# Performance work log

Hardware: AMD Instinct MI355X
Metric: run time of the kernel (lower is better)

Reference implementation:

```python
import jax, jax.numpy as jnp
import numpy as np

# NTU-25 joint groupings (0-indexed)
BODY_GROUP = [np.array([5,6,7,8,22,23])-1, np.array([9,10,11,12,24,25])-1,
              np.array([13,14,15,16])-1, np.array([17,18,19,20])-1,
              np.array([1,2,3,4,21])-1]
PART_GROUP = [np.array([1,2,21])-1, np.array([3,4])-1, np.array([5,6,7])-1,
              np.array([8,22,23])-1, np.array([9,10,11])-1, np.array([12,24,25])-1,
              np.array([13,14])-1, np.array([15,16])-1, np.array([17,18])-1,
              np.array([19,20])-1]

def _corr_joints(parts):
    num_joints = max(max(p) for p in parts) + 1
    res = []
    for i in range(num_joints):
        for j, p in enumerate(parts):
            if i in p:
                res.append(j)
                break
    return np.asarray(res, dtype=np.int32)

JOINTS_PART = _corr_joints(PART_GROUP)  # [25] -> part id in [0,10)
JOINTS_BODY = _corr_joints(BODY_GROUP)  # [25] -> body id in [0,5)

N, C, T, V, S = 64, 96, 128, 25, 3

def setup_inputs() -> dict:
    key = jax.random.key(0)
    ks = jax.random.split(key, 10)
    x = jax.random.normal(ks[0], (N, C, T, V), jnp.float32)
    p_att = jax.random.normal(ks[1], (N, S, 10, 10), jnp.float32)
    b_att = jax.random.normal(ks[2], (N, S, 5, 5), jnp.float32)
    w_in = jax.random.normal(ks[3], (3 * C, C), jnp.float32) * (1.0 / np.sqrt(C))
    b_in = jax.random.normal(ks[4], (3 * C,), jnp.float32) * 0.01
    w_ff = jax.random.normal(ks[5], (C, C), jnp.float32) * (1.0 / np.sqrt(C))
    b_ff = jax.random.normal(ks[6], (C,), jnp.float32) * 0.01
    bn_gamma = jnp.ones((C,), jnp.float32)
    bn_beta = jnp.zeros((C,), jnp.float32)
    bn_mean = jnp.zeros((C,), jnp.float32)
    bn_var = jnp.ones((C,), jnp.float32)
    return {"x": x, "p_att": p_att, "b_att": b_att, "w_in": w_in, "b_in": b_in,
            "w_ff": w_ff, "b_ff": b_ff, "bn_gamma": bn_gamma, "bn_beta": bn_beta,
            "bn_mean": bn_mean, "bn_var": bn_var}

def reference(x, p_att, b_att, w_in, b_in, w_ff, b_ff, bn_gamma, bn_beta, bn_mean, bn_var):
    n, c, t, v = x.shape
    s = S
    mid = c // s
    jp = jnp.asarray(JOINTS_PART)
    jb = jnp.asarray(JOINTS_BODY)
    # 1x1 conv -> QKV: [N, 3C, T, V] viewed as [N, 3, S, mid, T, V]
    qkv = jnp.einsum('nctv,oc->notv', x, w_in) + b_in[None, :, None, None]
    qkv = qkv.reshape(n, 3, s, mid, t, v)
    q, k, val = qkv[:, 0], qkv[:, 1], qkv[:, 2]
    att = jnp.tanh(jnp.einsum('nsctu,nsctv->nsuv', q, k) / (mid * t))
    # structured gather of part/body biases to joint-level [N,S,V,V]
    pp = p_att[:, :, jp[:, None], jp[None, :]]
    bb = b_att[:, :, jb[:, None], jb[None, :]]
    att = att + pp + bb
    y = jnp.einsum('nsuv,nsctv->nsctu', att, val).reshape(n, c, t, v)
    # ff_nets: 1x1 conv + BatchNorm (eval mode, running stats)
    y = jnp.einsum('nctv,oc->notv', y, w_ff) + b_ff[None, :, None, None]
    inv = bn_gamma / jnp.sqrt(bn_var + 1e-5)
    y = (y - bn_mean[None, :, None, None]) * inv[None, :, None, None] + bn_beta[None, :, None, None]
    return jax.nn.leaky_relu(x + y, 0.1)
```

## Files before the change

kernel.cpp:

```cpp
#include <hip/hip_runtime.h>
#include <cmath>

#define NN 64
#define CC 96
#define TT 128
#define VV 25
#define SS 3
#define TB 4
#define NTB (TT/TB)
#define ROWS (TB*VV)
#define XTROWS 112

#define XTP 104
#define XFP 104
#define QKP 200
#define VP  132
#define YP  104

typedef __attribute__((ext_vector_type(8))) __bf16 bf16x8;
typedef __attribute__((ext_vector_type(4))) float f32x4;

#define MFMA16(a,b,c) __builtin_amdgcn_mfma_f32_16x16x32_bf16((a),(b),(c),0,0,0)

__constant__ int JP[25] = {0,0,1,1,2,2,2,3,4,4,4,5,6,6,7,7,8,8,9,9,0,3,3,5,5};
__constant__ int JB[25] = {4,4,4,4,0,0,0,0,1,1,1,1,2,2,2,2,3,3,3,3,4,0,0,1,1};

__device__ inline unsigned short f2b(float f) {
  unsigned int u = __float_as_uint(f);
  u += 0x7fffu + ((u >> 16) & 1u);
  return (unsigned short)(u >> 16);
}
__device__ inline bf16x8 ldbf8(const unsigned short* p) {
  union { uint4 u; bf16x8 b; } z;
  z.u = *(const uint4*)p;
  return z.b;
}
__device__ inline f32x4 fz() {
  f32x4 z; z[0] = 0.f; z[1] = 0.f; z[2] = 0.f; z[3] = 0.f; return z;
}

__global__ __launch_bounds__(256) void k0(
    const float* __restrict__ w_in, const float* __restrict__ w_ff,
    const float* __restrict__ b_ff, const float* __restrict__ gam,
    const float* __restrict__ bet, const float* __restrict__ mea,
    const float* __restrict__ var,
    unsigned short* __restrict__ wbin, unsigned short* __restrict__ wbff,
    float* __restrict__ scsh)
{
  int i = blockIdx.x * 256 + threadIdx.x;
  if (i < 288 * 96) wbin[i] = f2b(w_in[i]);
  if (i < 96 * 96)  wbff[i] = f2b(w_ff[i]);
  if (i < 96) {
    float sc = gam[i] * rsqrtf(var[i] + 1e-5f);
    scsh[i]      = sc;
    scsh[96 + i] = (b_ff[i] - mea[i]) * sc + bet[i];
  }
}

__device__ inline void stageA(const float* __restrict__ xb,
                              unsigned short* __restrict__ xf, int tid)
{
  for (int e = tid; e < CC * (ROWS / 4); e += 256) {
    int i4 = e % (ROWS / 4), c = e / (ROWS / 4);
    float4 v = *(const float4*)&xb[(size_t)c * (TT * VV) + i4 * 4];
    ushort4 h;
    h.x = f2b(v.x); h.y = f2b(v.y); h.z = f2b(v.z); h.w = f2b(v.w);
    *(ushort4*)&xf[c * XFP + i4 * 4] = h;
  }
}
__device__ inline void stageB(const unsigned short* __restrict__ xf,
                              unsigned short* __restrict__ xT,
                              unsigned short* __restrict__ xwp, int tid)
{
  for (int e = tid; e < ROWS * (CC / 4); e += 256) {
    int i = e % ROWS, c4 = e / ROWS;
    ushort4 h;
    h.x = xf[(c4 * 4 + 0) * XFP + i];
    h.y = xf[(c4 * 4 + 1) * XFP + i];
    h.z = xf[(c4 * 4 + 2) * XFP + i];
    h.w = xf[(c4 * 4 + 3) * XFP + i];
    *(ushort4*)&xT[i * XTP + c4 * 4] = h;
    int dt = i / VV, v = i - dt * VV;
    *(ushort4*)&xwp[(size_t)(dt * 32 + v) * 96 + c4 * 4] = h;
  }
}

__global__ __launch_bounds__(256, 2) void k1(
    const float* __restrict__ x, const unsigned short* __restrict__ wbin,
    const float* __restrict__ b_in, float* __restrict__ partG,
    unsigned short* __restrict__ xw)
{
  __shared__ __align__(16) unsigned short xT[XTROWS * XTP];
  __shared__ __align__(16) unsigned short qk[XTROWS * QKP];
  __shared__ float bL[192];
  unsigned short* xf = qk;

  const int tid  = threadIdx.x;
  const int wid  = tid >> 6, lane = tid & 63;
  const int lrow = lane & 15;
  const int lk8  = (lane >> 4) << 3;
  const int ldr4 = (lane >> 4) << 2;
  const int tb = blockIdx.x & (NTB - 1);
  const int n  = blockIdx.x >> 5;
  const int t0 = tb * TB;

  const float* xb = x + (size_t)n * CC * TT * VV + (size_t)t0 * VV;
  unsigned short* xwp = xw + (size_t)(n * TT + t0) * 32 * 96;

  stageA(xb, xf, tid);
  if (tid < 192) bL[tid] = b_in[tid];
  __syncthreads();
  stageB(xf, xT, xwp, tid);
  __syncthreads();

  f32x4 acc[3][7];
  #pragma unroll
  for (int i = 0; i < 3; ++i)
    #pragma unroll
    for (int nf = 0; nf < 7; ++nf) acc[i][nf] = fz();

  #pragma unroll
  for (int ks = 0; ks < 3; ++ks) {
    bf16x8 a[3];
    #pragma unroll
    for (int i = 0; i < 3; ++i)
      a[i] = ldbf8(&wbin[((wid * 3 + i) * 16 + lrow) * 96 + ks * 32 + lk8]);
    #pragma unroll
    for (int nf = 0; nf < 7; ++nf) {
      bf16x8 b = ldbf8(&xT[(nf * 16 + lrow) * XTP + ks * 32 + lk8]);
      #pragma unroll
      for (int i = 0; i < 3; ++i)
        acc[i][nf] = MFMA16(a[i], b, acc[i][nf]);
    }
  }
  #pragma unroll
  for (int i = 0; i < 3; ++i) {
    int ob = (wid * 3 + i) * 16 + ldr4;
    float4 bb = *(const float4*)&bL[ob];
    #pragma unroll
    for (int nf = 0; nf < 7; ++nf) {
      int col = nf * 16 + lrow;
      ushort4 h;
      h.x = f2b(acc[i][nf][0] + bb.x);
      h.y = f2b(acc[i][nf][1] + bb.y);
      h.z = f2b(acc[i][nf][2] + bb.z);
      h.w = f2b(acc[i][nf][3] + bb.w);
      *(ushort4*)&qk[col * QKP + ob] = h;
    }
  }
  __syncthreads();

  if (wid < 3) {
    const int s = wid;
    f32x4 g[2][2];
    g[0][0] = fz(); g[0][1] = fz(); g[1][0] = fz(); g[1][1] = fz();
    #pragma unroll
    for (int dt = 0; dt < TB; ++dt) {
      int r0 = dt * VV;
      bf16x8 a0 = ldbf8(&qk[(r0 + lrow) * QKP + s * 32 + lk8]);
      bf16x8 a1 = ldbf8(&qk[(r0 + 16 + lrow) * QKP + s * 32 + lk8]);
      bf16x8 b0 = ldbf8(&qk[(r0 + lrow) * QKP + 96 + s * 32 + lk8]);
      bf16x8 b1 = ldbf8(&qk[(r0 + 16 + lrow) * QKP + 96 + s * 32 + lk8]);
      g[0][0] = MFMA16(a0, b0, g[0][0]);
      g[0][1] = MFMA16(a0, b1, g[0][1]);
      g[1][0] = MFMA16(a1, b0, g[1][0]);
      g[1][1] = MFMA16(a1, b1, g[1][1]);
    }
    float* pg = partG + ((size_t)tb * (NN * SS) + (n * SS + s)) * (VV * VV);
    #pragma unroll
    for (int mi = 0; mi < 2; ++mi)
      #pragma unroll
      for (int ni = 0; ni < 2; ++ni)
        #pragma unroll
        for (int r = 0; r < 4; ++r) {
          int u = mi * 16 + ldr4 + r, v = ni * 16 + lrow;
          if (u < VV && v < VV) pg[u * VV + v] = g[mi][ni][r];
        }
  }
}

__global__ __launch_bounds__(256) void k2(
    const float* __restrict__ partG, const float* __restrict__ p_att,
    const float* __restrict__ b_att, unsigned short* __restrict__ att)
{
  const int ns = blockIdx.x;
  for (int e = threadIdx.x; e < 1024; e += 256) {
    int u = e >> 5, v = e & 31;
    float a = 0.f;
    if (u < VV && v < VV) {
      float g = 0.f;
      #pragma unroll 4
      for (int tb = 0; tb < NTB; ++tb)
        g += partG[((size_t)tb * (NN * SS) + ns) * (VV * VV) + u * VV + v];
      a = tanhf(g * (1.0f / 4096.0f))
        + p_att[(size_t)ns * 100 + JP[u] * 10 + JP[v]]
        + b_att[(size_t)ns * 25  + JB[u] * 5  + JB[v]];
    }
    att[(size_t)ns * 1024 + e] = f2b(a);
  }
}

__global__ __launch_bounds__(256, 2) void k3(
    const float* __restrict__ x, const unsigned short* __restrict__ xw,
    const unsigned short* __restrict__ wbin,
    const unsigned short* __restrict__ wbff,
    const float* __restrict__ b_in, const float* __restrict__ scsh,
    const unsigned short* __restrict__ att, float* __restrict__ out)
{
  __shared__ __align__(16) unsigned short val[96 * VP];
  unsigned short* yL = val;

  const int tid  = threadIdx.x;
  const int wid  = tid >> 6, lane = tid & 63;
  const int lrow = lane & 15;
  const int lk8  = (lane >> 4) << 3;
  const int ldr4 = (lane >> 4) << 2;
  const int tb = blockIdx.x & (NTB - 1);
  const int n  = blockIdx.x >> 5;
  const int t0 = tb * TB;

  const unsigned short* xwn = xw + (size_t)(n * TT + t0) * 32 * 96;

  f32x4 vacc[2][6];
  #pragma unroll
  for (int m = 0; m < 2; ++m)
    #pragma unroll
    for (int of = 0; of < 6; ++of) vacc[m][of] = fz();

  #pragma unroll
  for (int ks = 0; ks < 3; ++ks) {
    bf16x8 bw[6];
    #pragma unroll
    for (int of = 0; of < 6; ++of)
      bw[of] = ldbf8(&wbin[(192 + of * 16 + lrow) * 96 + ks * 32 + lk8]);
    #pragma unroll
    for (int m = 0; m < 2; ++m) {
      bf16x8 a = ldbf8(&xwn[(size_t)((wid + m * 4) * 16 + lrow) * 96 + ks * 32 + lk8]);
      #pragma unroll
      for (int of = 0; of < 6; ++of)
        vacc[m][of] = MFMA16(a, bw[of], vacc[m][of]);
    }
  }
  float bv[6];
  #pragma unroll
  for (int of = 0; of < 6; ++of) bv[of] = b_in[192 + of * 16 + lrow];

  #pragma unroll
  for (int m = 0; m < 2; ++m) {
    int i0 = (wid + m * 4) * 16 + ldr4;
    int v0 = i0 & 31;
    #pragma unroll
    for (int of = 0; of < 6; ++of) {
      int cout = of * 16 + lrow;
      ushort4 h;
      h.x = (v0 + 0 < VV) ? f2b(vacc[m][of][0] + bv[of]) : (unsigned short)0;
      h.y = (v0 + 1 < VV) ? f2b(vacc[m][of][1] + bv[of]) : (unsigned short)0;
      h.z = (v0 + 2 < VV) ? f2b(vacc[m][of][2] + bv[of]) : (unsigned short)0;
      h.w = (v0 + 3 < VV) ? f2b(vacc[m][of][3] + bv[of]) : (unsigned short)0;
      *(ushort4*)&val[cout * VP + i0] = h;
    }
  }
  __syncthreads();

  const unsigned short* attn = att + (size_t)n * SS * 1024;
  f32x4 pacc[3][2][2];
  #pragma unroll
  for (int s = 0; s < 3; ++s)
    #pragma unroll
    for (int mi = 0; mi < 2; ++mi)
      #pragma unroll
      for (int uf = 0; uf < 2; ++uf) pacc[s][mi][uf] = fz();

  #pragma unroll
  for (int s = 0; s < 3; ++s) {
    bf16x8 av[2], bu[2];
    #pragma unroll
    for (int mi = 0; mi < 2; ++mi)
      av[mi] = ldbf8(&val[(s * 32 + mi * 16 + lrow) * VP + wid * 32 + lk8]);
    #pragma unroll
    for (int uf = 0; uf < 2; ++uf)
      bu[uf] = ldbf8(&attn[s * 1024 + (uf * 16 + lrow) * 32 + lk8]);
    #pragma unroll
    for (int mi = 0; mi < 2; ++mi)
      #pragma unroll
      for (int uf = 0; uf < 2; ++uf)
        pacc[s][mi][uf] = MFMA16(av[mi], bu[uf], pacc[s][mi][uf]);
  }
  __syncthreads();

  #pragma unroll
  for (int s = 0; s < 3; ++s)
    #pragma unroll
    for (int mi = 0; mi < 2; ++mi)
      #pragma unroll
      for (int uf = 0; uf < 2; ++uf) {
        int u = uf * 16 + lrow;
        if (u < VV) {
          int c0 = s * 32 + mi * 16 + ldr4;
          ushort4 h;
          h.x = f2b(pacc[s][mi][uf][0]);
          h.y = f2b(pacc[s][mi][uf][1]);
          h.z = f2b(pacc[s][mi][uf][2]);
          h.w = f2b(pacc[s][mi][uf][3]);
          *(ushort4*)&yL[(wid * VV + u) * YP + c0] = h;
        }
      }
  __syncthreads();

  #pragma unroll
  for (int rep = 0; rep < 2; ++rep) {
    int nf = wid + rep * 4;
    if (nf < 7) {
      f32x4 facc[6];
      #pragma unroll
      for (int of = 0; of < 6; ++of) facc[of] = fz();
      #pragma unroll
      for (int ks = 0; ks < 3; ++ks) {
        bf16x8 by = ldbf8(&yL[(nf * 16 + lrow) * YP + ks * 32 + lk8]);
        #pragma unroll
        for (int of = 0; of < 6; ++of) {
          bf16x8 aw = ldbf8(&wbff[(of * 16 + lrow) * 96 + ks * 32 + lk8]);
          facc[of] = MFMA16(aw, by, facc[of]);
        }
      }
      int i = nf * 16 + lrow;
      if (i < ROWS) {
        size_t base = (size_t)n * CC * (TT * VV) + (size_t)t0 * VV + i;
        #pragma unroll
        for (int of = 0; of < 6; ++of) {
          int o0 = of * 16 + ldr4;
          float4 sc = *(const float4*)&scsh[o0];
          float4 sh = *(const float4*)&scsh[96 + o0];
          const float* scp = (const float*)&sc;
          const float* shp = (const float*)&sh;
          #pragma unroll
          for (int r = 0; r < 4; ++r) {
            size_t idx = base + (size_t)(o0 + r) * (TT * VV);
            float z = facc[of][r] * scp[r] + shp[r] + x[idx];
            out[idx] = (z >= 0.f) ? z : 0.1f * z;
          }
        }
      }
    }
  }
}

extern "C" void kernel_launch(void* const* d_in, const int* in_sizes, int n_in,
                              void* d_out, int out_size, void* d_ws, size_t ws_size,
                              hipStream_t stream)
{
  const float* x     = (const float*)d_in[0];
  const float* p_att = (const float*)d_in[1];
  const float* b_att = (const float*)d_in[2];
  const float* w_in  = (const float*)d_in[3];
  const float* b_in  = (const float*)d_in[4];
  const float* w_ff  = (const float*)d_in[5];
  const float* b_ff  = (const float*)d_in[6];
  const float* gam   = (const float*)d_in[7];
  const float* bet   = (const float*)d_in[8];
  const float* mea   = (const float*)d_in[9];
  const float* var   = (const float*)d_in[10];
  float* out = (float*)d_out;

  char* ws = (char*)d_ws;
  unsigned short* wbin = (unsigned short*)ws;
  unsigned short* wbff = wbin + 288 * 96;
  unsigned short* attw = wbff + 96 * 96;
  float* scsh  = (float*)(ws + 466944);
  float* partG = (float*)(ws + 467712);
  unsigned short* xw = (unsigned short*)(ws + 15827712);

  k0<<<108, 256, 0, stream>>>(w_in, w_ff, b_ff, gam, bet, mea, var,
                              wbin, wbff, scsh);
  k1<<<NN * NTB, 256, 0, stream>>>(x, wbin, b_in, partG, xw);
  k2<<<NN * SS, 256, 0, stream>>>(partG, p_att, b_att, attw);
  k3<<<NN * NTB, 256, 0, stream>>>(x, xw, wbin, wbff, b_in, scsh, attw, out);
}
```

Measured before the change: 133.0 us.

## Recompute bf16 x transpose in k3 instead of round-tripping through workspace

k1 no longer writes a padded bf16 transposed copy of x to global workspace. k3 now reloads fp32 x, converts and transposes it in LDS itself, and stages the value and feed-forward weights plus the bias and scale/shift vectors in shared memory. This removes a global write and read of the intermediate and replaces scattered global weight loads with LDS reads. In exchange k3 reads x twice and uses much more LDS per block, which may lower occupancy.

```diff
diff --git a/kernel.cpp b/kernel.cpp
--- a/kernel.cpp
+++ b/kernel.cpp
@@ -14,8 +14,10 @@
 #define XTP 104
 #define XFP 104
 #define QKP 200
-#define VP  132
+#define X3P 104
+#define VP  136
 #define YP  104
+#define WLP 104
 
 typedef __attribute__((ext_vector_type(8))) __bf16 bf16x8;
 typedef __attribute__((ext_vector_type(4))) float f32x4;
@@ -68,10 +70,29 @@
     *(ushort4*)&xf[c * XFP + i4 * 4] = h;
   }
 }
-__device__ inline void stageB(const unsigned short* __restrict__ xf,
-                              unsigned short* __restrict__ xT,
-                              unsigned short* __restrict__ xwp, int tid)
-{
+
+__global__ __launch_bounds__(256, 2) void k1(
+    const float* __restrict__ x, const unsigned short* __restrict__ wbin,
+    const float* __restrict__ b_in, float* __restrict__ partG)
+{
+  __shared__ __align__(16) unsigned short xT[XTROWS * XTP];
+  __shared__ __align__(16) unsigned short qk[XTROWS * QKP];
+  __shared__ float bL[192];
+  unsigned short* xf = qk;
+
+  const int tid  = threadIdx.x;
+  const int wid  = tid >> 6, lane = tid & 63;
+  const int lrow = lane & 15;
+  const int lk8  = (lane >> 4) << 3;
+  const int ldr4 = (lane >> 4) << 2;
+  const int tb = blockIdx.x & (NTB - 1);
+  const int n  = blockIdx.x >> 5;
+  const int t0 = tb * TB;
+
+  const float* xb = x + (size_t)n * CC * TT * VV + (size_t)t0 * VV;
+  stageA(xb, xf, tid);
+  if (tid < 192) bL[tid] = b_in[tid];
+  __syncthreads();
   for (int e = tid; e < ROWS * (CC / 4); e += 256) {
     int i = e % ROWS, c4 = e / ROWS;
     ushort4 h;
@@ -80,37 +101,7 @@
     h.z = xf[(c4 * 4 + 2) * XFP + i];
     h.w = xf[(c4 * 4 + 3) * XFP + i];
     *(ushort4*)&xT[i * XTP + c4 * 4] = h;
-    int dt = i / VV, v = i - dt * VV;
-    *(ushort4*)&xwp[(size_t)(dt * 32 + v) * 96 + c4 * 4] = h;
-  }
-}
-
-__global__ __launch_bounds__(256, 2) void k1(
-    const float* __restrict__ x, const unsigned short* __restrict__ wbin,
-    const float* __restrict__ b_in, float* __restrict__ partG,
-    unsigned short* __restrict__ xw)
-{
-  __shared__ __align__(16) unsigned short xT[XTROWS * XTP];
-  __shared__ __align__(16) unsigned short qk[XTROWS * QKP];
-  __shared__ float bL[192];
-  unsigned short* xf = qk;
-
-  const int tid  = threadIdx.x;
-  const int wid  = tid >> 6, lane = tid & 63;
-  const int lrow = lane & 15;
-  const int lk8  = (lane >> 4) << 3;
-  const int ldr4 = (lane >> 4) << 2;
-  const int tb = blockIdx.x & (NTB - 1);
-  const int n  = blockIdx.x >> 5;
-  const int t0 = tb * TB;
-
-  const float* xb = x + (size_t)n * CC * TT * VV + (size_t)t0 * VV;
-  unsigned short* xwp = xw + (size_t)(n * TT + t0) * 32 * 96;
-
-  stageA(xb, xf, tid);
-  if (tid < 192) bL[tid] = b_in[tid];
-  __syncthreads();
-  stageB(xf, xT, xwp, tid);
+  }
   __syncthreads();
 
   f32x4 acc[3][7];
@@ -201,14 +192,18 @@
 }
 
 __global__ __launch_bounds__(256, 2) void k3(
-    const float* __restrict__ x, const unsigned short* __restrict__ xw,
-    const unsigned short* __restrict__ wbin,
+    const float* __restrict__ x, const unsigned short* __restrict__ wbin,
     const unsigned short* __restrict__ wbff,
     const float* __restrict__ b_in, const float* __restrict__ scsh,
     const unsigned short* __restrict__ att, float* __restrict__ out)
 {
+  __shared__ __align__(16) unsigned short xT32[128 * X3P];
   __shared__ __align__(16) unsigned short val[96 * VP];
-  unsigned short* yL = val;
+  __shared__ __align__(16) unsigned short wL[96 * WLP];
+  __shared__ float bvL[96];
+  __shared__ float scshL[192];
+  unsigned short* xf = val;
+  unsigned short* yL = xT32;
 
   const int tid  = threadIdx.x;
   const int wid  = tid >> 6, lane = tid & 63;
@@ -219,7 +214,35 @@
   const int n  = blockIdx.x >> 5;
   const int t0 = tb * TB;
 
-  const unsigned short* xwn = xw + (size_t)(n * TT + t0) * 32 * 96;
+  const float* xb = x + (size_t)n * CC * TT * VV + (size_t)t0 * VV;
+
+  stageA(xb, xf, tid);
+  for (int e = tid; e < 96 * 12; e += 256) {
+    int r = e / 12, q = e % 12;
+    *(uint4*)&wL[r * WLP + q * 8] =
+        *(const uint4*)&wbin[(size_t)(192 + r) * 96 + q * 8];
+  }
+  for (int e = tid; e < 28 * 13; e += 256) {
+    int pr = e / 13, q = e % 13;
+    int row = (pr / 7) * 32 + 25 + (pr % 7);
+    uint4 z; z.x = 0u; z.y = 0u; z.z = 0u; z.w = 0u;
+    *(uint4*)&xT32[row * X3P + q * 8] = z;
+  }
+  if (tid < 96)  bvL[tid]   = b_in[192 + tid];
+  if (tid < 192) scshL[tid] = scsh[tid];
+  __syncthreads();
+
+  for (int e = tid; e < ROWS * (CC / 4); e += 256) {
+    int i = e % ROWS, c4 = e / ROWS;
+    int row = (i / VV) * 32 + (i % VV);
+    ushort4 h;
+    h.x = xf[(c4 * 4 + 0) * XFP + i];
+    h.y = xf[(c4 * 4 + 1) * XFP + i];
+    h.z = xf[(c4 * 4 + 2) * XFP + i];
+    h.w = xf[(c4 * 4 + 3) * XFP + i];
+    *(ushort4*)&xT32[row * X3P + c4 * 4] = h;
+  }
+  __syncthreads();
 
   f32x4 vacc[2][6];
   #pragma unroll
@@ -232,10 +255,10 @@
     bf16x8 bw[6];
     #pragma unroll
     for (int of = 0; of < 6; ++of)
-      bw[of] = ldbf8(&wbin[(192 + of * 16 + lrow) * 96 + ks * 32 + lk8]);
+      bw[of] = ldbf8(&wL[(of * 16 + lrow) * WLP + ks * 32 + lk8]);
     #pragma unroll
     for (int m = 0; m < 2; ++m) {
-      bf16x8 a = ldbf8(&xwn[(size_t)((wid + m * 4) * 16 + lrow) * 96 + ks * 32 + lk8]);
+      bf16x8 a = ldbf8(&xT32[((wid + m * 4) * 16 + lrow) * X3P + ks * 32 + lk8]);
       #pragma unroll
       for (int of = 0; of < 6; ++of)
         vacc[m][of] = MFMA16(a, bw[of], vacc[m][of]);
@@ -243,7 +266,7 @@
   }
   float bv[6];
   #pragma unroll
-  for (int of = 0; of < 6; ++of) bv[of] = b_in[192 + of * 16 + lrow];
+  for (int of = 0; of < 6; ++of) bv[of] = bvL[of * 16 + lrow];
 
   #pragma unroll
   for (int m = 0; m < 2; ++m) {
@@ -262,6 +285,12 @@
   }
   __syncthreads();
 
+  for (int e = tid; e < 96 * 12; e += 256) {
+    int r = e / 12, q = e % 12;
+    *(uint4*)&wL[r * WLP + q * 8] =
+        *(const uint4*)&wbff[(size_t)r * 96 + q * 8];
+  }
+
   const unsigned short* attn = att + (size_t)n * SS * 1024;
   f32x4 pacc[3][2][2];
   #pragma unroll
@@ -286,7 +315,6 @@
       for (int uf = 0; uf < 2; ++uf)
         pacc[s][mi][uf] = MFMA16(av[mi], bu[uf], pacc[s][mi][uf]);
   }
-  __syncthreads();
 
   #pragma unroll
   for (int s = 0; s < 3; ++s)
@@ -319,7 +347,7 @@
         bf16x8 by = ldbf8(&yL[(nf * 16 + lrow) * YP + ks * 32 + lk8]);
         #pragma unroll
         for (int of = 0; of < 6; ++of) {
-          bf16x8 aw = ldbf8(&wbff[(of * 16 + lrow) * 96 + ks * 32 + lk8]);
+          bf16x8 aw = ldbf8(&wL[(of * 16 + lrow) * WLP + ks * 32 + lk8]);
           facc[of] = MFMA16(aw, by, facc[of]);
         }
       }
@@ -329,8 +357,8 @@
         #pragma unroll
         for (int of = 0; of < 6; ++of) {
           int o0 = of * 16 + ldr4;
-          float4 sc = *(const float4*)&scsh[o0];
-          float4 sh = *(const float4*)&scsh[96 + o0];
+          float4 sc = *(const float4*)&scshL[o0];
+          float4 sh = *(const float4*)&scshL[96 + o0];
           const float* scp = (const float*)&sc;
           const float* shp = (const float*)&sh;
           #pragma unroll
@@ -368,11 +396,10 @@
   unsigned short* attw = wbff + 96 * 96;
   float* scsh  = (float*)(ws + 466944);
   float* partG = (float*)(ws + 467712);
-  unsigned short* xw = (unsigned short*)(ws + 15827712);
 
   k0<<<108, 256, 0, stream>>>(w_in, w_ff, b_ff, gam, bet, mea, var,
                               wbin, wbff, scsh);
-  k1<<<NN * NTB, 256, 0, stream>>>(x, wbin, b_in, partG, xw);
+  k1<<<NN * NTB, 256, 0, stream>>>(x, wbin, b_in, partG);
   k2<<<NN * SS, 256, 0, stream>>>(partG, p_att, b_att, attw);
-  k3<<<NN * NTB, 256, 0, stream>>>(x, xw, wbin, wbff, b_in, scsh, attw, out);
-}
+  k3<<<NN * NTB, 256, 0, stream>>>(x, wbin, wbff, b_in, scsh, attw, out);
+}
```

Result: faster. 130.1 us (-2.2%).

## Compute V projection in k1 and write bf16 values instead of transposed x

Applied to the files above, without the earlier changes.

The V projection moves from k3 into k1, which already holds x in shared memory. k1 now writes the finished bf16 V tensor, padded to 32 joints, to workspace instead of a transposed copy of x. k3 reads V straight from global memory, stages the ff weights in LDS, and raises its occupancy hint to 3 blocks. The intent is to shorten k3 and remove the repeated V GEMM there, at the cost of larger LDS use and a longer k1, where the QKV GEMM now also covers padding rows (8 fragments instead of 7).

```diff
diff --git a/kernel.cpp b/kernel.cpp
--- a/kernel.cpp
+++ b/kernel.cpp
@@ -9,13 +9,12 @@
 #define TB 4
 #define NTB (TT/TB)
 #define ROWS (TB*VV)
-#define XTROWS 112
-
-#define XTP 104
+
 #define XFP 104
+#define X3P 104
 #define QKP 200
-#define VP  132
 #define YP  104
+#define WLP 104
 
 typedef __attribute__((ext_vector_type(8))) __bf16 bf16x8;
 typedef __attribute__((ext_vector_type(4))) float f32x4;
@@ -57,43 +56,16 @@
   }
 }
 
-__device__ inline void stageA(const float* __restrict__ xb,
-                              unsigned short* __restrict__ xf, int tid)
-{
-  for (int e = tid; e < CC * (ROWS / 4); e += 256) {
-    int i4 = e % (ROWS / 4), c = e / (ROWS / 4);
-    float4 v = *(const float4*)&xb[(size_t)c * (TT * VV) + i4 * 4];
-    ushort4 h;
-    h.x = f2b(v.x); h.y = f2b(v.y); h.z = f2b(v.z); h.w = f2b(v.w);
-    *(ushort4*)&xf[c * XFP + i4 * 4] = h;
-  }
-}
-__device__ inline void stageB(const unsigned short* __restrict__ xf,
-                              unsigned short* __restrict__ xT,
-                              unsigned short* __restrict__ xwp, int tid)
-{
-  for (int e = tid; e < ROWS * (CC / 4); e += 256) {
-    int i = e % ROWS, c4 = e / ROWS;
-    ushort4 h;
-    h.x = xf[(c4 * 4 + 0) * XFP + i];
-    h.y = xf[(c4 * 4 + 1) * XFP + i];
-    h.z = xf[(c4 * 4 + 2) * XFP + i];
-    h.w = xf[(c4 * 4 + 3) * XFP + i];
-    *(ushort4*)&xT[i * XTP + c4 * 4] = h;
-    int dt = i / VV, v = i - dt * VV;
-    *(ushort4*)&xwp[(size_t)(dt * 32 + v) * 96 + c4 * 4] = h;
-  }
-}
-
 __global__ __launch_bounds__(256, 2) void k1(
     const float* __restrict__ x, const unsigned short* __restrict__ wbin,
     const float* __restrict__ b_in, float* __restrict__ partG,
-    unsigned short* __restrict__ xw)
-{
-  __shared__ __align__(16) unsigned short xT[XTROWS * XTP];
-  __shared__ __align__(16) unsigned short qk[XTROWS * QKP];
+    unsigned short* __restrict__ val_ws)
+{
+  __shared__ __align__(16) unsigned short xT32[128 * X3P];
+  __shared__ __align__(16) unsigned short qk[128 * QKP];
   __shared__ float bL[192];
-  unsigned short* xf = qk;
+  unsigned short* xf   = qk;
+  unsigned short* valL = qk;
 
   const int tid  = threadIdx.x;
   const int wid  = tid >> 6, lane = tid & 63;
@@ -105,19 +77,39 @@
   const int t0 = tb * TB;
 
   const float* xb = x + (size_t)n * CC * TT * VV + (size_t)t0 * VV;
-  unsigned short* xwp = xw + (size_t)(n * TT + t0) * 32 * 96;
-
-  stageA(xb, xf, tid);
+  for (int e = tid; e < CC * (ROWS / 4); e += 256) {
+    int i4 = e % (ROWS / 4), c = e / (ROWS / 4);
+    float4 v = *(const float4*)&xb[(size_t)c * (TT * VV) + i4 * 4];
+    ushort4 h;
+    h.x = f2b(v.x); h.y = f2b(v.y); h.z = f2b(v.z); h.w = f2b(v.w);
+    *(ushort4*)&xf[c * XFP + i4 * 4] = h;
+  }
+  for (int e = tid; e < 28 * 13; e += 256) {
+    int pr = e / 13, q = e % 13;
+    int row = (pr / 7) * 32 + 25 + (pr % 7);
+    uint4 z; z.x = 0u; z.y = 0u; z.z = 0u; z.w = 0u;
+    *(uint4*)&xT32[row * X3P + q * 8] = z;
+  }
   if (tid < 192) bL[tid] = b_in[tid];
   __syncthreads();
-  stageB(xf, xT, xwp, tid);
-  __syncthreads();
-
-  f32x4 acc[3][7];
+
+  for (int e = tid; e < ROWS * (CC / 4); e += 256) {
+    int i = e % ROWS, c4 = e / ROWS;
+    int row = (i / VV) * 32 + (i % VV);
+    ushort4 h;
+    h.x = xf[(c4 * 4 + 0) * XFP + i];
+    h.y = xf[(c4 * 4 + 1) * XFP + i];
+    h.z = xf[(c4 * 4 + 2) * XFP + i];
+    h.w = xf[(c4 * 4 + 3) * XFP + i];
+    *(ushort4*)&xT32[row * X3P + c4 * 4] = h;
+  }
+  __syncthreads();
+
+  f32x4 acc[3][8];
   #pragma unroll
   for (int i = 0; i < 3; ++i)
     #pragma unroll
-    for (int nf = 0; nf < 7; ++nf) acc[i][nf] = fz();
+    for (int nf = 0; nf < 8; ++nf) acc[i][nf] = fz();
 
   #pragma unroll
   for (int ks = 0; ks < 3; ++ks) {
@@ -126,8 +118,8 @@
     for (int i = 0; i < 3; ++i)
       a[i] = ldbf8(&wbin[((wid * 3 + i) * 16 + lrow) * 96 + ks * 32 + lk8]);
     #pragma unroll
-    for (int nf = 0; nf < 7; ++nf) {
-      bf16x8 b = ldbf8(&xT[(nf * 16 + lrow) * XTP + ks * 32 + lk8]);
+    for (int nf = 0; nf < 8; ++nf) {
+      bf16x8 b = ldbf8(&xT32[(nf * 16 + lrow) * X3P + ks * 32 + lk8]);
       #pragma unroll
       for (int i = 0; i < 3; ++i)
         acc[i][nf] = MFMA16(a[i], b, acc[i][nf]);
@@ -138,7 +130,7 @@
     int ob = (wid * 3 + i) * 16 + ldr4;
     float4 bb = *(const float4*)&bL[ob];
     #pragma unroll
-    for (int nf = 0; nf < 7; ++nf) {
+    for (int nf = 0; nf < 8; ++nf) {
       int col = nf * 16 + lrow;
       ushort4 h;
       h.x = f2b(acc[i][nf][0] + bb.x);
@@ -150,13 +142,33 @@
   }
   __syncthreads();
 
+  f32x4 vacc[2][6];
+  #pragma unroll
+  for (int m = 0; m < 2; ++m)
+    #pragma unroll
+    for (int of = 0; of < 6; ++of) vacc[m][of] = fz();
+  #pragma unroll
+  for (int ks = 0; ks < 3; ++ks) {
+    bf16x8 bw[6];
+    #pragma unroll
+    for (int of = 0; of < 6; ++of)
+      bw[of] = ldbf8(&wbin[(192 + of * 16 + lrow) * 96 + ks * 32 + lk8]);
+    #pragma unroll
+    for (int m = 0; m < 2; ++m) {
+      bf16x8 a = ldbf8(&xT32[((wid + m * 4) * 16 + lrow) * X3P + ks * 32 + lk8]);
+      #pragma unroll
+      for (int of = 0; of < 6; ++of)
+        vacc[m][of] = MFMA16(a, bw[of], vacc[m][of]);
+    }
+  }
+
   if (wid < 3) {
     const int s = wid;
     f32x4 g[2][2];
     g[0][0] = fz(); g[0][1] = fz(); g[1][0] = fz(); g[1][1] = fz();
     #pragma unroll
     for (int dt = 0; dt < TB; ++dt) {
-      int r0 = dt * VV;
+      int r0 = dt * 32;
       bf16x8 a0 = ldbf8(&qk[(r0 + lrow) * QKP + s * 32 + lk8]);
       bf16x8 a1 = ldbf8(&qk[(r0 + 16 + lrow) * QKP + s * 32 + lk8]);
       bf16x8 b0 = ldbf8(&qk[(r0 + lrow) * QKP + 96 + s * 32 + lk8]);
@@ -176,6 +188,33 @@
           int u = mi * 16 + ldr4 + r, v = ni * 16 + lrow;
           if (u < VV && v < VV) pg[u * VV + v] = g[mi][ni][r];
         }
+  }
+  __syncthreads();
+
+  float bv[6];
+  #pragma unroll
+  for (int of = 0; of < 6; ++of) bv[of] = b_in[192 + of * 16 + lrow];
+  #pragma unroll
+  for (int m = 0; m < 2; ++m) {
+    int i0 = (wid + m * 4) * 16 + ldr4;
+    #pragma unroll
+    for (int of = 0; of < 6; ++of) {
+      int cout = of * 16 + lrow;
+      ushort4 h;
+      h.x = f2b(vacc[m][of][0] + bv[of]);
+      h.y = f2b(vacc[m][of][1] + bv[of]);
+      h.z = f2b(vacc[m][of][2] + bv[of]);
+      h.w = f2b(vacc[m][of][3] + bv[of]);
+      *(ushort4*)&valL[cout * 128 + i0] = h;
+    }
+  }
+  __syncthreads();
+
+  for (int e = tid; e < 1536; e += 256) {
+    int c4 = e & 3, t = (e >> 2) & 3, cout = e >> 4;
+    uint4 w = *(uint4*)&valL[cout * 128 + t * 32 + c4 * 8];
+    if (c4 == 3) { w.x &= 0xFFFFu; w.y = 0u; w.z = 0u; w.w = 0u; }
+    *(uint4*)&val_ws[(((size_t)(n * 96 + cout)) * TT + (t0 + t)) * 32 + c4 * 8] = w;
   }
 }
 
@@ -200,15 +239,13 @@
   }
 }
 
-__global__ __launch_bounds__(256, 2) void k3(
-    const float* __restrict__ x, const unsigned short* __restrict__ xw,
-    const unsigned short* __restrict__ wbin,
-    const unsigned short* __restrict__ wbff,
-    const float* __restrict__ b_in, const float* __restrict__ scsh,
+__global__ __launch_bounds__(256, 3) void k3(
+    const float* __restrict__ x, const unsigned short* __restrict__ val_ws,
+    const unsigned short* __restrict__ wbff, const float* __restrict__ scsh,
     const unsigned short* __restrict__ att, float* __restrict__ out)
 {
-  __shared__ __align__(16) unsigned short val[96 * VP];
-  unsigned short* yL = val;
+  __shared__ __align__(16) unsigned short yL[112 * YP];
+  __shared__ __align__(16) unsigned short wL[96 * WLP];
 
   const int tid  = threadIdx.x;
   const int wid  = tid >> 6, lane = tid & 63;
@@ -218,49 +255,12 @@
   const int tb = blockIdx.x & (NTB - 1);
   const int n  = blockIdx.x >> 5;
   const int t0 = tb * TB;
-
-  const unsigned short* xwn = xw + (size_t)(n * TT + t0) * 32 * 96;
-
-  f32x4 vacc[2][6];
-  #pragma unroll
-  for (int m = 0; m < 2; ++m)
-    #pragma unroll
-    for (int of = 0; of < 6; ++of) vacc[m][of] = fz();
-
-  #pragma unroll
-  for (int ks = 0; ks < 3; ++ks) {
-    bf16x8 bw[6];
-    #pragma unroll
-    for (int of = 0; of < 6; ++of)
-      bw[of] = ldbf8(&wbin[(192 + of * 16 + lrow) * 96 + ks * 32 + lk8]);
-    #pragma unroll
-    for (int m = 0; m < 2; ++m) {
-      bf16x8 a = ldbf8(&xwn[(size_t)((wid + m * 4) * 16 + lrow) * 96 + ks * 32 + lk8]);
-      #pragma unroll
-      for (int of = 0; of < 6; ++of)
-        vacc[m][of] = MFMA16(a, bw[of], vacc[m][of]);
-    }
-  }
-  float bv[6];
-  #pragma unroll
-  for (int of = 0; of < 6; ++of) bv[of] = b_in[192 + of * 16 + lrow];
-
-  #pragma unroll
-  for (int m = 0; m < 2; ++m) {
-    int i0 = (wid + m * 4) * 16 + ldr4;
-    int v0 = i0 & 31;
-    #pragma unroll
-    for (int of = 0; of < 6; ++of) {
-      int cout = of * 16 + lrow;
-      ushort4 h;
-      h.x = (v0 + 0 < VV) ? f2b(vacc[m][of][0] + bv[of]) : (unsigned short)0;
-      h.y = (v0 + 1 < VV) ? f2b(vacc[m][of][1] + bv[of]) : (unsigned short)0;
-      h.z = (v0 + 2 < VV) ? f2b(vacc[m][of][2] + bv[of]) : (unsigned short)0;
-      h.w = (v0 + 3 < VV) ? f2b(vacc[m][of][3] + bv[of]) : (unsigned short)0;
-      *(ushort4*)&val[cout * VP + i0] = h;
-    }
-  }
-  __syncthreads();
+  const int t  = t0 + wid;
+
+  for (int e = tid; e < 96 * 12; e += 256) {
+    int r = e / 12, q = e % 12;
+    *(uint4*)&wL[r * WLP + q * 8] = *(const uint4*)&wbff[(size_t)r * 96 + q * 8];
+  }
 
   const unsigned short* attn = att + (size_t)n * SS * 1024;
   f32x4 pacc[3][2][2];
@@ -275,8 +275,10 @@
   for (int s = 0; s < 3; ++s) {
     bf16x8 av[2], bu[2];
     #pragma unroll
-    for (int mi = 0; mi < 2; ++mi)
-      av[mi] = ldbf8(&val[(s * 32 + mi * 16 + lrow) * VP + wid * 32 + lk8]);
+    for (int mi = 0; mi < 2; ++mi) {
+      int c = s * 32 + mi * 16 + lrow;
+      av[mi] = ldbf8(&val_ws[(((size_t)(n * 96 + c)) * TT + t) * 32 + lk8]);
+    }
     #pragma unroll
     for (int uf = 0; uf < 2; ++uf)
       bu[uf] = ldbf8(&attn[s * 1024 + (uf * 16 + lrow) * 32 + lk8]);
@@ -286,7 +288,6 @@
       for (int uf = 0; uf < 2; ++uf)
         pacc[s][mi][uf] = MFMA16(av[mi], bu[uf], pacc[s][mi][uf]);
   }
-  __syncthreads();
 
   #pragma unroll
   for (int s = 0; s < 3; ++s)
@@ -319,7 +320,7 @@
         bf16x8 by = ldbf8(&yL[(nf * 16 + lrow) * YP + ks * 32 + lk8]);
         #pragma unroll
         for (int of = 0; of < 6; ++of) {
-          bf16x8 aw = ldbf8(&wbff[(of * 16 + lrow) * 96 + ks * 32 + lk8]);
+          bf16x8 aw = ldbf8(&wL[(of * 16 + lrow) * WLP + ks * 32 + lk8]);
           facc[of] = MFMA16(aw, by, facc[of]);
         }
       }
@@ -368,11 +369,11 @@
   unsigned short* attw = wbff + 96 * 96;
   float* scsh  = (float*)(ws + 466944);
   float* partG = (float*)(ws + 467712);
-  unsigned short* xw = (unsigned short*)(ws + 15827712);
+  unsigned short* val_ws = (unsigned short*)(ws + 15827712);
 
   k0<<<108, 256, 0, stream>>>(w_in, w_ff, b_ff, gam, bet, mea, var,
                               wbin, wbff, scsh);
-  k1<<<NN * NTB, 256, 0, stream>>>(x, wbin, b_in, partG, xw);
+  k1<<<NN * NTB, 256, 0, stream>>>(x, wbin, b_in, partG, val_ws);
   k2<<<NN * SS, 256, 0, stream>>>(partG, p_att, b_att, attw);
-  k3<<<NN * NTB, 256, 0, stream>>>(x, xw, wbin, wbff, b_in, scsh, attw, out);
-}
+  k3<<<NN * NTB, 256, 0, stream>>>(x, val_ws, wbff, scsh, attw, out);
+}
```

Result: no change. 130.9 us (-1.6%).
